# Optimization experiments

Measured on AMD Instinct MI355X. Metric: run time of the kernel, lower is better.

The kernel has to match this reference:

```python
import jax, jax.numpy as jnp
import numpy as np

V, E, H, K, VD, NH, FS, NL = 32000, 512, 512, 512, 512, 8, 2048, 6
B, MEM, SLEN = 256, 70, 11
MAXLEN = 71
THRESH = 1.0 - 0.1
EPS = 1e-6


def _timing_signal(length, channels):
    # Faithful to _gen_timing_signal (min_timescale=1, max_timescale=1e4)
    position = np.arange(length, dtype=np.float32)
    num_ts = channels // 2
    log_inc = np.log(1e4) / (num_ts - 1)
    inv_ts = np.exp(np.arange(num_ts, dtype=np.float32) * -log_inc)
    scaled = position[:, None] * inv_ts[None, :]
    sig = np.concatenate([np.sin(scaled), np.cos(scaled)], axis=1)
    return jnp.asarray(sig.reshape(1, length, channels), dtype=jnp.float32)

TIME_SIG = _timing_signal(MAXLEN, H)   # [1, 71, H]
POS_SIG = _timing_signal(NL, H)        # [1, NL, H]


def layer_norm(x, g, b):
    mu = x.mean(-1, keepdims=True)
    sd = x.std(-1, keepdims=True, ddof=1)  # torch std is unbiased
    return g * (x - mu) / (sd + EPS) + b


def conv1d(x, w, b):
    # x: [B,L,Cin]; w: torch layout [Cout,Cin,3]; 'both' padding -> same length
    y = jax.lax.conv_general_dilated(x, jnp.transpose(w, (2, 1, 0)), (1,), [(1, 1)],
                                     dimension_numbers=('NWC', 'WIO', 'NWC'))
    return y + b


def mha(x, wq, wk, wv, wo):
    Bx, L, _ = x.shape
    dk, dv = K // NH, VD // NH
    q = (x @ wq).reshape(Bx, L, NH, dk).transpose(0, 2, 1, 3) * dk ** -0.5
    k = (x @ wk).reshape(Bx, L, NH, dk).transpose(0, 2, 1, 3)
    v = (x @ wv).reshape(Bx, L, NH, dv).transpose(0, 2, 1, 3)
    a = jax.nn.softmax(jnp.einsum('bhqd,bhkd->bhqk', q, k), axis=-1)
    ctx = jnp.einsum('bhqk,bhkd->bhqd', a, v).transpose(0, 2, 1, 3).reshape(Bx, L, VD)
    return ctx @ wo


def enc_layer(x, p):
    xn = layer_norm(x, p['ln1_g'], p['ln1_b'])
    x = x + mha(xn, p['wq'], p['wk'], p['wv'], p['wo'])
    xn = layer_norm(x, p['ln2_g'], p['ln2_b'])
    y = conv1d(jax.nn.relu(conv1d(xn, p['c1_w'], p['c1_b'])), p['c2_w'], p['c2_b'])
    return x + y


def act_encode(x, p):
    Bx, L, _ = x.shape
    hp = jnp.zeros((Bx, L), x.dtype)
    rem = jnp.zeros((Bx, L), x.dtype)
    nu = jnp.zeros((Bx, L), x.dtype)
    prev = jnp.zeros_like(x)

    def step(carry, t):
        state, prev, hp, rem, nu = carry
        active = jnp.any((hp < THRESH) & (nu < NL))  # while-loop condition
        s = state + TIME_SIG[:, :L, :] + POS_SIG[:, t, :][:, None, :]
        pr = jax.nn.sigmoid(s @ p['p_w'] + p['p_b'])[..., 0]  # [B,L]
        still = (hp < 1.0).astype(x.dtype)
        tot = hp + pr * still
        new_halted = (tot > THRESH).astype(x.dtype) * still
        still2 = (tot <= THRESH).astype(x.dtype) * still
        hp2 = hp + pr * still2
        rem2 = rem + new_halted * (1.0 - hp2)
        hp2 = hp2 + new_halted * rem2
        nu2 = nu + still2 + new_halted
        uw = (pr * still2 + new_halted * rem2)[..., None]
        s2 = enc_layer(s, p)
        prev2 = s2 * uw + prev * (1.0 - uw)
        new = (s2, prev2, hp2, rem2, nu2)
        carry = jax.tree_util.tree_map(lambda a, b: jnp.where(active, b, a), carry, new)
        return carry, None

    (_, prev, hp, rem, nu), _ = jax.lax.scan(step, (x, prev, hp, rem, nu), jnp.arange(NL))
    return prev, rem, nu


def setup_inputs() -> dict:
    key = jax.random.key(0)
    ks = jax.random.split(key, 16)
    s = 0.02
    emb = jax.random.normal(ks[0], (V, E), jnp.float32) * s
    emb = emb.at[0].set(0.0)  # padding_idx=0
    return {
        'story': jax.random.randint(ks[1], (B, MEM, SLEN), 0, V),
        'query': jax.random.randint(ks[2], (B, SLEN), 0, V),
        'emb': emb,
        'mask_p': jnp.ones((11, E), jnp.float32),
        'proj_w': jax.random.normal(ks[3], (E, H), jnp.float32) * s,
        'ln1_g': jnp.ones((H,), jnp.float32), 'ln1_b': jnp.zeros((H,), jnp.float32),
        'wq': jax.random.normal(ks[4], (H, K), jnp.float32) * s,
        'wk': jax.random.normal(ks[5], (H, K), jnp.float32) * s,
        'wv': jax.random.normal(ks[6], (H, VD), jnp.float32) * s,
        'wo': jax.random.normal(ks[7], (VD, H), jnp.float32) * s,
        'c1_w': jax.random.normal(ks[8], (FS, H, 3), jnp.float32) * s,
        'c1_b': jnp.zeros((FS,), jnp.float32),
        'c2_w': jax.random.normal(ks[9], (H, FS, 3), jnp.float32) * s,
        'c2_b': jnp.zeros((H,), jnp.float32),
        'ln2_g': jnp.ones((H,), jnp.float32), 'ln2_b': jnp.zeros((H,), jnp.float32),
        'p_w': jax.random.normal(ks[10], (H, 1), jnp.float32) * s,
        'p_b': jnp.ones((1,), jnp.float32),  # bias init to 1 as in ACT_basic
        'out_b': jnp.zeros((V,), jnp.float32),
    }


def reference(story, query, emb, mask_p, proj_w, ln1_g, ln1_b, wq, wk, wv, wo,
              c1_w, c1_b, c2_w, c2_b, ln2_g, ln2_b, p_w, p_b, out_b):
    p = dict(ln1_g=ln1_g, ln1_b=ln1_b, wq=wq, wk=wk, wv=wv, wo=wo,
             c1_w=c1_w, c1_b=c1_b, c2_w=c2_w, c2_b=c2_b,
             ln2_g=ln2_g, ln2_b=ln2_b, p_w=p_w, p_b=p_b)
    S = story.shape[2]
    e = emb[story]                                         # [B,M,S,E]
    embed_story = jnp.sum(e * mask_p[:S][None, None], 2)   # [B,M,E]
    qe = emb[query]                                        # [B,S,E]
    embed_query = jnp.sum(qe[:, None] * mask_p[:query.shape[1]], 2)  # [B,1,E]
    x = jnp.concatenate([embed_story, embed_query], axis=1)          # [B,M+1,E]
    h = x @ proj_w  # proj_flag path (embedding_size == hidden_size)
    logit, rem, nu = act_encode(h, p)
    pooled = jnp.sum(logit, axis=1) / logit.shape[1]
    a_hat = pooled @ emb.T + out_b  # tied output weights
    return a_hat, jax.nn.softmax(a_hat, axis=1), rem, nu
```

## Files before the change

### kernel.cpp

```cpp
#include <hip/hip_runtime.h>
#include <hip/hip_bf16.h>
#include <math.h>


typedef unsigned short ushort_t;
using short8   = __attribute__((ext_vector_type(8))) short;
using floatx4  = __attribute__((ext_vector_type(4))) float;
using ushort4v = __attribute__((ext_vector_type(4))) unsigned short;

#define B_   256
#define L_   71
#define H_   512
#define M_   (B_*L_)
#define MH_  9088
#define FS_  2048
#define V_   32000
#define NH_  8
#define DK_  64

#define ATS  68
#define SST  72

__device__ inline ushort_t f2bf_rne(float f) {
    unsigned u = __float_as_uint(f);
    return (ushort_t)((u + 0x7FFFu + ((u >> 16) & 1u)) >> 16);
}

__device__ __forceinline__ void gload16(const void* g, void* l)
{
    __builtin_amdgcn_global_load_lds(
        (__attribute__((address_space(1))) unsigned int*)(g),
        (__attribute__((address_space(3))) unsigned int*)(l),
        16, 0, 0);
}

template<int MODE>
__global__ __launch_bounds__(256) void gemm_conv(
    const ushort_t* __restrict__ AH, const ushort_t* __restrict__ AL,
    int lda, int rowA, int rowG,
    const ushort_t* __restrict__ Bh, const ushort_t* __restrict__ Bl,
    int N, const float* __restrict__ bias,
    ushort_t* __restrict__ CoutH, ushort_t* __restrict__ CoutL,
    float* __restrict__ Cpart, long partStride, int cLen)
{
    __shared__ __attribute__((aligned(16))) short Ahs[4608], Als[4608];
    __shared__ __attribute__((aligned(16))) short Bhs[6144], Bls[6144];

    const int tid  = threadIdx.x;
    const int w    = tid >> 6, lane = tid & 63;

    int bn, by, z;
    if (MODE == 1) {
        const int id = blockIdx.x;
        const int l  = (id & 7) * 142 + (id >> 3);
        const int gp = l >> 2;
        by = gp % 71;
        const int zz = gp / 71;
        z  = zz >> 1;
        bn = (zz & 1) * 4 + (l & 3);
    } else {
        bn = blockIdx.x; by = blockIdx.y; z = 0;
    }
    const int cBeg = z * cLen;
    const int bm = by << 7;

    const int srow = lane & 15, skc = lane >> 4;
    const long aOff0 = (long)(rowA + bm - 1 + (w    ) * 16 + srow) * lda + skc * 8;
    const long aOff1 = (long)(rowA + bm - 1 + (w + 4) * 16 + srow) * lda + skc * 8;
    const long aOff2 = (long)(rowA + bm - 1 + 128 + srow) * lda + skc * 8;
    const long ldb = 3L * lda;
    const long bOff0 = (long)(bn * 64 + ((w    ) & 3) * 16 + srow) * ldb + ((w    ) >> 2) * lda + skc * 8;
    const long bOff1 = (long)(bn * 64 + ((w + 4) & 3) * 16 + srow) * ldb + ((w + 4) >> 2) * lda + skc * 8;
    const long bOff2 = (long)(bn * 64 + ((w + 8) & 3) * 16 + srow) * ldb + ((w + 8) >> 2) * lda + skc * 8;

    const int quad = lane >> 4, mr = lane & 15;
    const int boffL = quad * 128 + mr * 8;
    int aoffs[2][3];
    bool am0[2], am2[2];
    #pragma unroll
    for (int i = 0; i < 2; i++) {
        #pragma unroll
        for (int d = 0; d < 3; d++) {
            const int s = w * 32 + i * 16 + mr + d;
            aoffs[i][d] = (s >> 4) * 512 + quad * 128 + (s & 15) * 8;
        }
        const int lm = (bm + w * 32 + i * 16 + mr + rowG) % 71;
        am0[i] = (lm == 0);
        am2[i] = (lm == 70);
    }

    floatx4 acc[2][4] = {};

    const int cEnd = cBeg + cLen;
    for (int c0 = cBeg; c0 < cEnd; c0 += 32) {
        __syncthreads();
        gload16(AH + aOff0 + c0, Ahs + (w    ) * 512);
        gload16(AH + aOff1 + c0, Ahs + (w + 4) * 512);
        gload16(AL + aOff0 + c0, Als + (w    ) * 512);
        gload16(AL + aOff1 + c0, Als + (w + 4) * 512);
        if (w == 0) {
            gload16(AH + aOff2 + c0, Ahs + 8 * 512);
            gload16(AL + aOff2 + c0, Als + 8 * 512);
        }
        gload16(Bh + bOff0 + c0, Bhs + (w    ) * 512);
        gload16(Bh + bOff1 + c0, Bhs + (w + 4) * 512);
        gload16(Bh + bOff2 + c0, Bhs + (w + 8) * 512);
        gload16(Bl + bOff0 + c0, Bls + (w    ) * 512);
        gload16(Bl + bOff1 + c0, Bls + (w + 4) * 512);
        gload16(Bl + bOff2 + c0, Bls + (w + 8) * 512);
        __syncthreads();

        #pragma unroll
        for (int d = 0; d < 3; d++) {
            short8 bhf[4], blf[4];
            #pragma unroll
            for (int j = 0; j < 4; j++) {
                bhf[j] = *(const short8*)(Bhs + (d * 4 + j) * 512 + boffL);
                blf[j] = *(const short8*)(Bls + (d * 4 + j) * 512 + boffL);
            }
            #pragma unroll
            for (int i = 0; i < 2; i++) {
                short8 a_h = *(const short8*)(Ahs + aoffs[i][d]);
                short8 a_l = *(const short8*)(Als + aoffs[i][d]);
                if (d == 0) { if (am0[i]) { a_h = (short8)0; a_l = (short8)0; } }
                if (d == 2) { if (am2[i]) { a_h = (short8)0; a_l = (short8)0; } }
                #pragma unroll
                for (int j = 0; j < 4; j++) {
                    acc[i][j] = __builtin_amdgcn_mfma_f32_16x16x32_bf16(a_h, bhf[j], acc[i][j], 0, 0, 0);
                    acc[i][j] = __builtin_amdgcn_mfma_f32_16x16x32_bf16(a_l, bhf[j], acc[i][j], 0, 0, 0);
                    acc[i][j] = __builtin_amdgcn_mfma_f32_16x16x32_bf16(a_h, blf[j], acc[i][j], 0, 0, 0);
                }
            }
        }
    }

    #pragma unroll
    for (int j = 0; j < 4; j++) {
        const int gcol = bn * 64 + j * 16 + mr;
        const float bv = (MODE == 0) ? bias[gcol] : 0.f;
        #pragma unroll
        for (int i = 0; i < 2; i++) {
            #pragma unroll
            for (int r = 0; r < 4; r++) {
                const int grow = bm + w * 32 + i * 16 + quad * 4 + r;
                float v = acc[i][j][r];
                if (MODE == 0) {
                    v = fmaxf(v + bv, 0.f);
                    const long cidx = (long)grow * N + gcol;
                    ushort_t h = f2bf_rne(v);
                    float hf = __uint_as_float(((unsigned)h) << 16);
                    CoutH[cidx] = h;
                    CoutL[cidx] = f2bf_rne(v - hf);
                } else {
                    Cpart[(long)z * partStride + (long)grow * N + gcol] = v;
                }
            }
        }
    }
}

template<int TN>
__global__ __launch_bounds__(256) void gemm_s(
    const ushort_t* __restrict__ AH, const ushort_t* __restrict__ AL,
    int lda, int rowA,
    const ushort_t* __restrict__ Bh, const ushort_t* __restrict__ Bl,
    int N, int K,
    const float* __restrict__ bias, const float* residual,
    float alpha, int rowC, int outMode,
    float* Cout, ushort_t* CoutH, ushort_t* CoutL)
{
    constexpr int AF = (TN == 128) ? 4 : 2;
    __shared__ __attribute__((aligned(16))) short Ahs[4096], Als[4096];
    __shared__ __attribute__((aligned(16))) short Bhs[TN * 32], Bls[TN * 32];

    const int tid  = threadIdx.x;
    const int w    = tid >> 6, lane = tid & 63;
    const int bm = blockIdx.y << 7, bn = blockIdx.x * TN;

    const int srow = lane & 15;
    const int skc  = lane >> 4;
    const int ra0  = w * 16 + srow;
    const int ra1  = ra0 + 64;
    const ushort_t* pAh0 = AH + (long)(bm + ra0 + rowA) * lda + skc * 8;
    const ushort_t* pAl0 = AL + (long)(bm + ra0 + rowA) * lda + skc * 8;
    const ushort_t* pAh1 = AH + (long)(bm + ra1 + rowA) * lda + skc * 8;
    const ushort_t* pAl1 = AL + (long)(bm + ra1 + rowA) * lda + skc * 8;
    const ushort_t* pBh0 = Bh + (long)(bn + ra0) * K + skc * 8;
    const ushort_t* pBl0 = Bl + (long)(bn + ra0) * K + skc * 8;
    const ushort_t* pBh1 = (TN == 128) ? (Bh + (long)(bn + ra1) * K + skc * 8) : nullptr;
    const ushort_t* pBl1 = (TN == 128) ? (Bl + (long)(bn + ra1) * K + skc * 8) : nullptr;

    const int quad = lane >> 4, mr = lane & 15;
    const int wrM   = (TN == 128) ? ((w >> 1) << 6) : (w << 5);
    const int wcN   = (TN == 128) ? ((w & 1) << 6) : 0;
    const int agrp0 = (TN == 128) ? ((w >> 1) << 2) : (w << 1);
    const int bgrp0 = (TN == 128) ? ((w & 1) << 2) : 0;
    const int foff  = quad * 128 + mr * 8;

    floatx4 acc[AF][4] = {};

    for (int k0 = 0; k0 < K; k0 += 32) {
        __syncthreads();
        gload16(pAh0 + k0, Ahs + w * 512);
        gload16(pAh1 + k0, Ahs + (w + 4) * 512);
        gload16(pAl0 + k0, Als + w * 512);
        gload16(pAl1 + k0, Als + (w + 4) * 512);
        if constexpr (TN == 128) {
            gload16(pBh0 + k0, Bhs + w * 512);
            gload16(pBh1 + k0, Bhs + (w + 4) * 512);
            gload16(pBl0 + k0, Bls + w * 512);
            gload16(pBl1 + k0, Bls + (w + 4) * 512);
        } else {
            gload16(pBh0 + k0, Bhs + w * 512);
            gload16(pBl0 + k0, Bls + w * 512);
        }
        __syncthreads();

        short8 ah[AF], al[AF], bh[4], bl[4];
        #pragma unroll
        for (int i = 0; i < AF; i++) {
            ah[i] = *(const short8*)(Ahs + (agrp0 + i) * 512 + foff);
            al[i] = *(const short8*)(Als + (agrp0 + i) * 512 + foff);
        }
        #pragma unroll
        for (int j = 0; j < 4; j++) {
            bh[j] = *(const short8*)(Bhs + (bgrp0 + j) * 512 + foff);
            bl[j] = *(const short8*)(Bls + (bgrp0 + j) * 512 + foff);
        }
        #pragma unroll
        for (int i = 0; i < AF; i++)
        #pragma unroll
        for (int j = 0; j < 4; j++) {
            acc[i][j] = __builtin_amdgcn_mfma_f32_16x16x32_bf16(ah[i], bh[j], acc[i][j], 0, 0, 0);
            acc[i][j] = __builtin_amdgcn_mfma_f32_16x16x32_bf16(al[i], bh[j], acc[i][j], 0, 0, 0);
            acc[i][j] = __builtin_amdgcn_mfma_f32_16x16x32_bf16(ah[i], bl[j], acc[i][j], 0, 0, 0);
        }
    }

    #pragma unroll
    for (int j = 0; j < 4; j++) {
        const int gcol = bn + wcN + j * 16 + mr;
        const float bv = bias ? bias[gcol] : 0.f;
        #pragma unroll
        for (int i = 0; i < AF; i++) {
            #pragma unroll
            for (int r = 0; r < 4; r++) {
                const int grow = bm + wrM + i * 16 + quad * 4 + r;
                const long crow = (long)grow + rowC;
                float v = acc[i][j][r] * alpha + bv;
                if (residual) v += residual[crow * N + gcol];
                const long cidx = crow * (long)N + gcol;
                if (outMode == 2) {
                    ushort_t h = f2bf_rne(v);
                    float hf = __uint_as_float(((unsigned)h) << 16);
                    CoutH[cidx] = h;
                    CoutL[cidx] = f2bf_rne(v - hf);
                } else {
                    Cout[cidx] = v;
                }
            }
        }
    }
}

__global__ __launch_bounds__(256) void conv2_reduce(
    const float* __restrict__ part, long partStride,
    const float* __restrict__ bias, float* __restrict__ trunk,
    float* __restrict__ prev, const float* __restrict__ uw, int rowC)
{
    const long n4 = (long)MH_ * H_ / 4;
    long i4 = (long)blockIdx.x * 256 + threadIdx.x;
    if (i4 >= n4) return;
    const long row  = i4 >> 7;
    const float4 p0 = ((const float4*)part)[i4];
    const float4 p1 = ((const float4*)(part + partStride))[i4];
    const float4 b4 = ((const float4*)bias)[i4 & 127];
    const long  ti  = (long)rowC * 128 + i4;
    float4 tv = ((const float4*)trunk)[ti];
    float4 v;
    v.x = p0.x + p1.x + b4.x + tv.x;
    v.y = p0.y + p1.y + b4.y + tv.y;
    v.z = p0.z + p1.z + b4.z + tv.z;
    v.w = p0.w + p1.w + b4.w + tv.w;
    ((float4*)trunk)[ti] = v;
    const float u = uw[rowC + row];
    float4 pv = ((const float4*)prev)[ti];
    pv.x = v.x * u + pv.x * (1.f - u);
    pv.y = v.y * u + pv.y * (1.f - u);
    pv.z = v.z * u + pv.z * (1.f - u);
    pv.w = v.w * u + pv.w * (1.f - u);
    ((float4*)prev)[ti] = pv;
}

__global__ __launch_bounds__(256) void sig_prep(float* __restrict__ T, float* __restrict__ P)
{
    int i = blockIdx.x * 256 + threadIdx.x;
    const int NT = 71 * 512;
    if (i >= NT + 6 * 512) return;
    int pos, c, idx;
    float* dst;
    if (i < NT) { pos = i >> 9; c = i & 511; dst = T; idx = i; }
    else        { int j = i - NT; pos = j >> 9; c = j & 511; dst = P; idx = j; }
    const float loginc = 0.036119766f;
    int jj = c & 255;
    float inv = expf(-(float)jj * loginc);
    float arg = (float)pos * inv;
    dst[idx] = (c < 256) ? sinf(arg) : cosf(arg);
}

__global__ __launch_bounds__(256) void gate_kernel(
    const float* __restrict__ hp, const float* __restrict__ nu, int* __restrict__ flag)
{
    int i = blockIdx.x * 256 + threadIdx.x;
    bool act = (i < M_) && (hp[i] < 0.9f) && (nu[i] < 6.0f);
    unsigned long long b = __ballot(act);
    if ((threadIdx.x & 63) == 0 && b) atomicOr(flag, 1);
}

__global__ __launch_bounds__(256) void s_pr_kernel(
    float* trunk, const float* __restrict__ Ttab, const float* __restrict__ Ptab,
    const float* __restrict__ p_w, const float* __restrict__ p_b,
    float* __restrict__ hp, float* __restrict__ rem, float* __restrict__ nu,
    float* __restrict__ uw, const int* __restrict__ flag, int t)
{
    const int row  = blockIdx.x * 4 + (threadIdx.x >> 6);
    const int lane = threadIdx.x & 63;
    const int l    = row % 71;
    float dot = 0.f;
    #pragma unroll
    for (int j = 0; j < 8; j++) {
        int c  = lane + 64 * j;
        float sv = trunk[(long)row * H_ + c] + Ttab[l * H_ + c] + Ptab[t * H_ + c];
        trunk[(long)row * H_ + c] = sv;
        dot += sv * p_w[c];
    }
    #pragma unroll
    for (int o = 32; o; o >>= 1) dot += __shfl_xor(dot, o);
    if (lane == 0) {
        if (flag[0]) {
            float pr = 1.f / (1.f + expf(-(dot + p_b[0])));
            float hp0 = hp[row], rem0 = rem[row], nu0 = nu[row];
            float still = (hp0 < 1.0f) ? 1.f : 0.f;
            float tot   = hp0 + pr * still;
            float nh    = ((tot > 0.9f) ? 1.f : 0.f) * still;
            float st2   = ((tot <= 0.9f) ? 1.f : 0.f) * still;
            float hp2   = hp0 + pr * st2;
            float rem2  = rem0 + nh * (1.f - hp2);
            hp2 += nh * rem2;
            hp[row] = hp2; rem[row] = rem2; nu[row] = nu0 + st2 + nh;
            uw[row] = pr * st2 + nh * rem2;
        } else {
            uw[row] = 0.f;
        }
    }
}

__global__ __launch_bounds__(256) void ln_kernel(
    const float* __restrict__ X, const float* __restrict__ g,
    const float* __restrict__ bb, ushort_t* __restrict__ outH,
    ushort_t* __restrict__ outL)
{
    const int row  = blockIdx.x * 4 + (threadIdx.x >> 6);
    const int lane = threadIdx.x & 63;
    const float* xr = X + (long)row * H_;
    float v[8];
    float s = 0.f;
    #pragma unroll
    for (int j = 0; j < 8; j++) { v[j] = xr[lane + 64 * j]; s += v[j]; }
    #pragma unroll
    for (int o = 32; o; o >>= 1) s += __shfl_xor(s, o);
    float mean = s * (1.f / 512.f);
    float q = 0.f;
    #pragma unroll
    for (int j = 0; j < 8; j++) { float d = v[j] - mean; q += d * d; }
    #pragma unroll
    for (int o = 32; o; o >>= 1) q += __shfl_xor(q, o);
    float sd  = sqrtf(q * (1.f / 511.f));
    float inv = 1.f / (sd + 1e-6f);
    #pragma unroll
    for (int j = 0; j < 8; j++) {
        int c = lane + 64 * j;
        float val = g[c] * (v[j] - mean) * inv + bb[c];
        ushort_t h = f2bf_rne(val);
        float hf = __uint_as_float(((unsigned)h) << 16);
        long idx = (long)row * H_ + c;
        outH[idx] = h;
        outL[idx] = f2bf_rne(val - hf);
    }
}

__global__ __launch_bounds__(256) void attn_kernel(
    const float* __restrict__ qkv, ushort_t* __restrict__ ctxH,
    ushort_t* __restrict__ ctxL)
{
    __shared__ __attribute__((aligned(16))) float qs[L_ * ATS];
    __shared__ __attribute__((aligned(16))) float ks[(L_ + 1) * ATS];
    __shared__ __attribute__((aligned(16))) float Ss[L_ * SST];
    __shared__ float rsum[L_ + 1];
    const int tid = threadIdx.x;
    const int b = blockIdx.x >> 3, h = blockIdx.x & 7;
    const long qbase = (long)b * L_ * 1536 + h * DK_;

    for (int idx = tid; idx < L_ * 16; idx += 256) {
        const int i = idx >> 4, s4 = idx & 15;
        const float4 qv = *(const float4*)(qkv + qbase + (long)i * 1536 + 4 * s4);
        const float4 kv = *(const float4*)(qkv + qbase + 512 + (long)i * 1536 + 4 * s4);
        *(float4*)(qs + i * ATS + 4 * s4) = qv;
        *(float4*)(ks + i * ATS + 4 * s4) = kv;
    }
    if (tid < 16) {
        float4 zz = {0.f, 0.f, 0.f, 0.f};
        *(float4*)(ks + 71 * ATS + 4 * tid) = zz;
    }
    __syncthreads();

    for (int item = tid; item < 18 * L_; item += 256) {
        const int jq = item / 71, i = item - jq * 71;
        const float* qr = qs + i * ATS;
        const float* k0 = ks + (4 * jq) * ATS;
        float s0 = 0.f, s1 = 0.f, s2 = 0.f, s3 = 0.f;
        #pragma unroll
        for (int s4 = 0; s4 < 16; s4++) {
            const float4 qv = *(const float4*)(qr + 4 * s4);
            const float4 k0v = *(const float4*)(k0 + 4 * s4);
            const float4 k1v = *(const float4*)(k0 + ATS + 4 * s4);
            const float4 k2v = *(const float4*)(k0 + 2 * ATS + 4 * s4);
            const float4 k3v = *(const float4*)(k0 + 3 * ATS + 4 * s4);
            s0 += qv.x * k0v.x + qv.y * k0v.y + qv.z * k0v.z + qv.w * k0v.w;
            s1 += qv.x * k1v.x + qv.y * k1v.y + qv.z * k1v.z + qv.w * k1v.w;
            s2 += qv.x * k2v.x + qv.y * k2v.y + qv.z * k2v.z + qv.w * k2v.w;
            s3 += qv.x * k3v.x + qv.y * k3v.y + qv.z * k3v.z + qv.w * k3v.w;
        }
        float4 sv; sv.x = s0; sv.y = s1; sv.z = s2; sv.w = s3;
        *(float4*)(Ss + i * SST + 4 * jq) = sv;
    }
    __syncthreads();

    for (int idx = tid; idx < L_ * 16; idx += 256) {
        const int i = idx >> 4, s4 = idx & 15;
        *(float4*)(ks + i * ATS + 4 * s4) =
            *(const float4*)(qkv + qbase + 1024 + (long)i * 1536 + 4 * s4);
    }

    {
        const int g = tid >> 2, r = tid & 3;
        #pragma unroll
        for (int half = 0; half < 2; half++) {
            const int row = g + half * 64;
            if (row < L_) {
                float4 vals[5];
                float mx = -1e30f;
                #pragma unroll
                for (int t = 0; t < 5; t++) {
                    const int q = r + 4 * t;
                    if (q < 18) {
                        float4 v = *(const float4*)(Ss + row * SST + 4 * q);
                        if (q == 17) v.w = -1e30f;
                        vals[t] = v;
                        mx = fmaxf(mx, fmaxf(fmaxf(v.x, v.y), fmaxf(v.z, v.w)));
                    }
                }
                mx = fmaxf(mx, __shfl_xor(mx, 1));
                mx = fmaxf(mx, __shfl_xor(mx, 2));
                float sm = 0.f;
                #pragma unroll
                for (int t = 0; t < 5; t++) {
                    const int q = r + 4 * t;
                    if (q < 18) {
                        float4 v = vals[t];
                        v.x = expf(v.x - mx); v.y = expf(v.y - mx);
                        v.z = expf(v.z - mx); v.w = expf(v.w - mx);
                        sm += v.x + v.y + v.z + v.w;
                        *(float4*)(Ss + row * SST + 4 * q) = v;
                    }
                }
                sm += __shfl_xor(sm, 1);
                sm += __shfl_xor(sm, 2);
                if (r == 0) rsum[row] = 1.f / sm;
            }
        }
    }
    __syncthreads();

    const long obase = (long)b * L_ * H_ + h * DK_;
    for (int item = tid; item < L_ * 16; item += 256) {
        const int i = item >> 4, dq = item & 15;
        const float* sr = Ss + i * SST;
        float ax = 0.f, ay = 0.f, az = 0.f, aw = 0.f;
        #pragma unroll
        for (int jq = 0; jq < 18; jq++) {
            const float4 sv = *(const float4*)(sr + 4 * jq);
            const float* v0 = ks + (4 * jq) * ATS + 4 * dq;
            const float4 va = *(const float4*)(v0);
            const float4 vb = *(const float4*)(v0 + ATS);
            const float4 vc = *(const float4*)(v0 + 2 * ATS);
            const float4 vd = *(const float4*)(v0 + 3 * ATS);
            ax += sv.x * va.x + sv.y * vb.x + sv.z * vc.x + sv.w * vd.x;
            ay += sv.x * va.y + sv.y * vb.y + sv.z * vc.y + sv.w * vd.y;
            az += sv.x * va.z + sv.y * vb.z + sv.z * vc.z + sv.w * vd.z;
            aw += sv.x * va.w + sv.y * vb.w + sv.z * vc.w + sv.w * vd.w;
        }
        const float rs = rsum[i];
        float o[4] = {ax * rs, ay * rs, az * rs, aw * rs};
        ushort4v hv, lv;
        #pragma unroll
        for (int c = 0; c < 4; c++) {
            ushort_t hh = f2bf_rne(o[c]);
            float hf = __uint_as_float(((unsigned)hh) << 16);
            hv[c] = hh;
            lv[c] = f2bf_rne(o[c] - hf);
        }
        const long oo = obase + (long)i * H_ + 4 * dq;
        *(ushort4v*)(ctxH + oo) = hv;
        *(ushort4v*)(ctxL + oo) = lv;
    }
}

__global__ __launch_bounds__(256) void embed_kernel(
    const int* __restrict__ story, const int* __restrict__ query,
    const float* __restrict__ emb, const float* __restrict__ mask,
    ushort_t* __restrict__ xH, ushort_t* __restrict__ xL)
{
    __shared__ int idx[11];
    const int row = blockIdx.x;
    const int b = row / 71, m = row % 71;
    const int tid = threadIdx.x;
    if (tid < 11)
        idx[tid] = (m < 70) ? story[((long)b * 70 + m) * 11 + tid]
                            : query[(long)b * 11 + tid];
    __syncthreads();
    for (int c = tid; c < H_; c += 256) {
        float acc = 0.f;
        #pragma unroll
        for (int s = 0; s < 11; s++)
            acc += emb[(long)idx[s] * H_ + c] * mask[s * H_ + c];
        ushort_t h = f2bf_rne(acc);
        float hf = __uint_as_float(((unsigned)h) << 16);
        long o = (long)row * H_ + c;
        xH[o] = h;
        xL[o] = f2bf_rne(acc - hf);
    }
}

__global__ __launch_bounds__(256) void wsplitT_kernel(
    const float* __restrict__ in, ushort_t* __restrict__ hi, ushort_t* __restrict__ lo,
    int R, int C, int rowOff, float scale)
{
    long i = (long)blockIdx.x * 256 + threadIdx.x;
    if (i < (long)R * C) {
        int r = (int)(i / C), c = (int)(i % C);
        float f = in[i] * scale;
        ushort_t h = f2bf_rne(f);
        float hf = __uint_as_float(((unsigned)h) << 16);
        hi[(long)(c + rowOff) * R + r] = h;
        lo[(long)(c + rowOff) * R + r] = f2bf_rne(f - hf);
    }
}

__global__ __launch_bounds__(256) void convw_split_kernel(
    const float* __restrict__ w, ushort_t* __restrict__ hi, ushort_t* __restrict__ lo,
    int N, int C)
{
    long i = (long)blockIdx.x * 256 + threadIdx.x;
    if (i < (long)N * C * 3) {
        int n = (int)(i / (3 * C));
        int r = (int)(i % (3 * C));
        int d = r / C, c = r % C;
        float f = w[((long)n * C + c) * 3 + d];
        ushort_t h = f2bf_rne(f);
        float hf = __uint_as_float(((unsigned)h) << 16);
        hi[i] = h;
        lo[i] = f2bf_rne(f - hf);
    }
}

__global__ __launch_bounds__(256) void esplit_kernel(
    const float* __restrict__ in, ushort_t* __restrict__ hi, ushort_t* __restrict__ lo,
    long n)
{
    long i = (long)blockIdx.x * 256 + threadIdx.x;
    if (i < n) {
        float f = in[i];
        ushort_t h = f2bf_rne(f);
        float hf = __uint_as_float(((unsigned)h) << 16);
        hi[i] = h;
        lo[i] = f2bf_rne(f - hf);
    }
}

__global__ __launch_bounds__(256) void zero_f32(float* __restrict__ p, long n)
{
    long i = (long)blockIdx.x * 256 + threadIdx.x;
    if (i < n) p[i] = 0.f;
}

__global__ __launch_bounds__(256) void pooled_kernel(
    const float* __restrict__ prev, ushort_t* __restrict__ pH, ushort_t* __restrict__ pL)
{
    int i = blockIdx.x * 256 + threadIdx.x;
    int b = i >> 9, c = i & 511;
    float s = 0.f;
    for (int l = 0; l < L_; l++) s += prev[((long)b * L_ + l) * H_ + c];
    float p = s / 71.0f;
    ushort_t h = f2bf_rne(p);
    float hf = __uint_as_float(((unsigned)h) << 16);
    pH[i] = h;
    pL[i] = f2bf_rne(p - hf);
}

__global__ __launch_bounds__(256) void softmax_kernel(
    const float* __restrict__ ah, float* __restrict__ out)
{
    __shared__ float red[256];
    const int b = blockIdx.x, tid = threadIdx.x;
    const float* a = ah + (long)b * V_;
    float mx = -1e30f;
    for (int i = tid; i < V_; i += 256) mx = fmaxf(mx, a[i]);
    red[tid] = mx; __syncthreads();
    for (int o = 128; o; o >>= 1) { if (tid < o) red[tid] = fmaxf(red[tid], red[tid + o]); __syncthreads(); }
    mx = red[0]; __syncthreads();
    float s = 0.f;
    for (int i = tid; i < V_; i += 256) s += expf(a[i] - mx);
    red[tid] = s; __syncthreads();
    for (int o = 128; o; o >>= 1) { if (tid < o) red[tid] += red[tid + o]; __syncthreads(); }
    float inv = 1.f / red[0];
    float* o_ = out + (long)b * V_;
    for (int i = tid; i < V_; i += 256) o_[i] = expf(a[i] - mx) * inv;
}

__global__ __launch_bounds__(256) void tails_kernel(
    const float* __restrict__ rem, const float* __restrict__ nu, float* __restrict__ out)
{
    int i = blockIdx.x * 256 + threadIdx.x;
    if (i < M_) {
        out[i] = rem[i];
        out[M_ + i] = nu[i];
    }
}

extern "C" void kernel_launch(void* const* d_in, const int* in_sizes, int n_in,
                              void* d_out, int out_size, void* d_ws, size_t ws_size,
                              hipStream_t stream)
{
    const int*   story  = (const int*)d_in[0];
    const int*   query  = (const int*)d_in[1];
    const float* emb    = (const float*)d_in[2];
    const float* mask_p = (const float*)d_in[3];
    const float* proj_w = (const float*)d_in[4];
    const float* ln1_g  = (const float*)d_in[5];
    const float* ln1_b  = (const float*)d_in[6];
    const float* wq     = (const float*)d_in[7];
    const float* wk     = (const float*)d_in[8];
    const float* wv     = (const float*)d_in[9];
    const float* wo     = (const float*)d_in[10];
    const float* c1_w   = (const float*)d_in[11];
    const float* c1_b   = (const float*)d_in[12];
    const float* c2_w   = (const float*)d_in[13];
    const float* c2_b   = (const float*)d_in[14];
    const float* ln2_g  = (const float*)d_in[15];
    const float* ln2_b  = (const float*)d_in[16];
    const float* p_w    = (const float*)d_in[17];
    const float* p_b    = (const float*)d_in[18];
    const float* out_b  = (const float*)d_in[19];
    float* outp = (float*)d_out;

    char* wsb = (char*)d_ws;
    size_t off = 0;
    auto alloc = [&](size_t bytes) -> void* {
        void* p = wsb + off;
        off = (off + bytes + 255) & ~(size_t)255;
        return p;
    };
    const long ROWE = (long)M_ * H_;

    float* trunkF = (float*)alloc(ROWE * 4);
    float* prevF  = (float*)alloc(ROWE * 4);
    char*  poolC  = (char*)alloc(4L * ROWE * 4);
    float* hpF    = (float*)alloc((long)M_ * 4 * 4 + 64);
    float* remF   = hpF + M_;
    float* nuF    = hpF + 2 * M_;
    float* uwF    = hpF + 3 * M_;
    int*   flags  = (int*)(hpF + 4 * M_);
    ushort_t* projH = (ushort_t*)alloc((long)H_ * H_ * 2);
    ushort_t* projL = (ushort_t*)alloc((long)H_ * H_ * 2);
    ushort_t* wqkvH = (ushort_t*)alloc((long)3 * H_ * H_ * 2);
    ushort_t* wqkvL = (ushort_t*)alloc((long)3 * H_ * H_ * 2);
    ushort_t* woH   = (ushort_t*)alloc((long)H_ * H_ * 2);
    ushort_t* woL   = (ushort_t*)alloc((long)H_ * H_ * 2);
    ushort_t* W1H   = (ushort_t*)alloc((long)FS_ * 3 * H_ * 2);
    ushort_t* W1L   = (ushort_t*)alloc((long)FS_ * 3 * H_ * 2);
    ushort_t* W2H   = (ushort_t*)alloc((long)H_ * 3 * FS_ * 2);
    ushort_t* W2L   = (ushort_t*)alloc((long)H_ * 3 * FS_ * 2);
    ushort_t* pooledH = (ushort_t*)alloc((long)B_ * H_ * 2);
    ushort_t* pooledL = (ushort_t*)alloc((long)B_ * H_ * 2);
    float* Ttab     = (float*)alloc((long)L_ * H_ * 4);
    float* Ptab     = (float*)alloc(6L * H_ * 4);

    ushort_t* xnH = (ushort_t*)poolC;
    ushort_t* xnL = xnH + ROWE;
    float* qkvF = (float*)(poolC + ROWE * 4);
    ushort_t* ctxH = xnH;
    ushort_t* ctxL = xnL;
    ushort_t* xn2H = (ushort_t*)poolC;
    ushort_t* xn2L = xn2H + ROWE;
    ushort_t* y1H  = (ushort_t*)(poolC + ROWE * 4);
    ushort_t* y1L  = y1H + (long)MH_ * FS_;
    float* partF   = (float*)(poolC + ROWE * 4 + (long)MH_ * FS_ * 4);
    ushort_t* xembH = (ushort_t*)poolC;
    ushort_t* xembL = xembH + ROWE;
    ushort_t* embH = (ushort_t*)poolC;
    ushort_t* embL = embH + (long)V_ * H_;

    dim3 blk(256);

    zero_f32<<<dim3((unsigned)((ROWE + 255) / 256)), blk, 0, stream>>>(prevF, ROWE);
    zero_f32<<<dim3((3 * M_ + 255) / 256), blk, 0, stream>>>(hpF, 3 * M_);
    zero_f32<<<dim3(1), blk, 0, stream>>>((float*)flags, 16);
    sig_prep<<<dim3(154), blk, 0, stream>>>(Ttab, Ptab);

    wsplitT_kernel<<<dim3(1024), blk, 0, stream>>>(proj_w, projH, projL, H_, H_, 0, 1.f);
    wsplitT_kernel<<<dim3(1024), blk, 0, stream>>>(wq, wqkvH, wqkvL, H_, H_, 0, 0.125f);
    wsplitT_kernel<<<dim3(1024), blk, 0, stream>>>(wk, wqkvH, wqkvL, H_, H_, 512, 1.f);
    wsplitT_kernel<<<dim3(1024), blk, 0, stream>>>(wv, wqkvH, wqkvL, H_, H_, 1024, 1.f);
    wsplitT_kernel<<<dim3(1024), blk, 0, stream>>>(wo, woH, woL, H_, H_, 0, 1.f);
    convw_split_kernel<<<dim3(12288), blk, 0, stream>>>(c1_w, W1H, W1L, FS_, H_);
    convw_split_kernel<<<dim3(12288), blk, 0, stream>>>(c2_w, W2H, W2L, H_, FS_);

    embed_kernel<<<dim3(M_), blk, 0, stream>>>(story, query, emb, mask_p, xembH, xembL);
    gemm_s<64><<<dim3(H_ / 64, M_ / 128), blk, 0, stream>>>(
        xembH, xembL, H_, 0, projH, projL, H_, H_,
        nullptr, nullptr, 1.f, 0, 0, trunkF, nullptr, nullptr);

    for (int t = 0; t < 6; t++) {
        gate_kernel<<<dim3(M_ / 256), blk, 0, stream>>>(hpF, nuF, flags + t);
        s_pr_kernel<<<dim3(M_ / 4), blk, 0, stream>>>(trunkF, Ttab, Ptab, p_w, p_b,
                                                      hpF, remF, nuF, uwF, flags + t, t);
        ln_kernel<<<dim3(M_ / 4), blk, 0, stream>>>(trunkF, ln1_g, ln1_b, xnH, xnL);
        gemm_s<128><<<dim3(1536 / 128, M_ / 128), blk, 0, stream>>>(
            xnH, xnL, H_, 0, wqkvH, wqkvL, 1536, H_,
            nullptr, nullptr, 1.f, 0, 0, qkvF, nullptr, nullptr);
        attn_kernel<<<dim3(B_ * NH_), blk, 0, stream>>>(qkvF, ctxH, ctxL);
        gemm_s<64><<<dim3(H_ / 64, M_ / 128), blk, 0, stream>>>(
            ctxH, ctxL, H_, 0, woH, woL, H_, H_,
            nullptr, trunkF, 1.f, 0, 0, trunkF, nullptr, nullptr);
        ln_kernel<<<dim3(M_ / 4), blk, 0, stream>>>(trunkF, ln2_g, ln2_b, xn2H, xn2L);
        for (int half = 0; half < 2; half++) {
            int ro = half * MH_;
            gemm_conv<0><<<dim3(32, 71), blk, 0, stream>>>(
                xn2H, xn2L, H_, ro, ro, W1H, W1L, FS_,
                c1_b, y1H, y1L, nullptr, 0, 512);
            gemm_conv<1><<<dim3(1136), blk, 0, stream>>>(
                y1H, y1L, FS_, 0, ro, W2H, W2L, H_,
                nullptr, nullptr, nullptr, partF, (long)MH_ * H_, 1024);
            conv2_reduce<<<dim3((unsigned)((long)MH_ * H_ / 4 / 256)), blk, 0, stream>>>(
                partF, (long)MH_ * H_, c2_b, trunkF, prevF, uwF, ro);
        }
    }

    pooled_kernel<<<dim3(B_ * H_ / 256), blk, 0, stream>>>(prevF, pooledH, pooledL);
    esplit_kernel<<<dim3(64000), blk, 0, stream>>>(emb, embH, embL, (long)V_ * H_);
    gemm_s<64><<<dim3(V_ / 64, B_ / 128), blk, 0, stream>>>(
        pooledH, pooledL, H_, 0, embH, embL, V_, H_,
        out_b, nullptr, 1.f, 0, 0, outp, nullptr, nullptr);
    softmax_kernel<<<dim3(B_), blk, 0, stream>>>(outp, outp + (long)B_ * V_);
    tails_kernel<<<dim3((M_ + 255) / 256), blk, 0, stream>>>(remF, nuF, outp + 2L * B_ * V_);
}
```

Baseline: 7.821 ms.

## Widen conv GEMM tile to 128x128 with 2x2 warp layout and XCD-aware block mapping

The conv-as-GEMM kernel now computes a 128-column output tile per block instead of 64, with waves laid out 2x2 (each wave covering 64 rows by 64 columns). This doubles the reuse of each staged A tile and halves the number of blocks, so less global and LDS traffic is spent per MFMA. Both modes get a 1D grid with an XCD-interleaved block-to-tile remap, which aims to improve L2 locality. In exchange, LDS for B doubles and the per-wave accumulators double, which may lower occupancy, and the smaller grid may fill the CUs less evenly.

```diff
diff --git a/kernel.cpp b/kernel.cpp
--- a/kernel.cpp
+++ b/kernel.cpp
@@ -44,7 +44,7 @@
     float* __restrict__ Cpart, long partStride, int cLen)
 {
     __shared__ __attribute__((aligned(16))) short Ahs[4608], Als[4608];
-    __shared__ __attribute__((aligned(16))) short Bhs[6144], Bls[6144];
+    __shared__ __attribute__((aligned(16))) short Bhs[12288], Bls[12288];
 
     const int tid  = threadIdx.x;
     const int w    = tid >> 6, lane = tid & 63;
@@ -52,44 +52,51 @@
     int bn, by, z;
     if (MODE == 1) {
         const int id = blockIdx.x;
+        const int l  = (id & 7) * 71 + (id >> 3);
+        by = l >> 3;
+        const int mem = l & 7;
+        z  = mem >> 2;
+        bn = mem & 3;
+    } else {
+        const int id = blockIdx.x;
         const int l  = (id & 7) * 142 + (id >> 3);
-        const int gp = l >> 2;
-        by = gp % 71;
-        const int zz = gp / 71;
-        z  = zz >> 1;
-        bn = (zz & 1) * 4 + (l & 3);
-    } else {
-        bn = blockIdx.x; by = blockIdx.y; z = 0;
+        by = l >> 4;
+        bn = l & 15;
+        z  = 0;
     }
     const int cBeg = z * cLen;
     const int bm = by << 7;
 
     const int srow = lane & 15, skc = lane >> 4;
+    const long ldb = 3L * lda;
     const long aOff0 = (long)(rowA + bm - 1 + (w    ) * 16 + srow) * lda + skc * 8;
     const long aOff1 = (long)(rowA + bm - 1 + (w + 4) * 16 + srow) * lda + skc * 8;
     const long aOff2 = (long)(rowA + bm - 1 + 128 + srow) * lda + skc * 8;
-    const long ldb = 3L * lda;
-    const long bOff0 = (long)(bn * 64 + ((w    ) & 3) * 16 + srow) * ldb + ((w    ) >> 2) * lda + skc * 8;
-    const long bOff1 = (long)(bn * 64 + ((w + 4) & 3) * 16 + srow) * ldb + ((w + 4) >> 2) * lda + skc * 8;
-    const long bOff2 = (long)(bn * 64 + ((w + 8) & 3) * 16 + srow) * ldb + ((w + 8) >> 2) * lda + skc * 8;
+    long bOffs[6];
+    #pragma unroll
+    for (int t = 0; t < 6; t++) {
+        const int u = w + 4 * t;
+        const int d = u >> 3, g = u & 7;
+        bOffs[t] = (long)(bn * 128 + g * 16 + srow) * ldb + (long)d * lda + skc * 8;
+    }
 
     const int quad = lane >> 4, mr = lane & 15;
-    const int boffL = quad * 128 + mr * 8;
-    int aoffs[2][3];
-    bool am0[2], am2[2];
-    #pragma unroll
-    for (int i = 0; i < 2; i++) {
+    const int wr = w >> 1, wc = w & 1;
+    int aoffs[4][3];
+    bool am0[4], am2[4];
+    #pragma unroll
+    for (int i = 0; i < 4; i++) {
         #pragma unroll
         for (int d = 0; d < 3; d++) {
-            const int s = w * 32 + i * 16 + mr + d;
+            const int s = wr * 64 + i * 16 + mr + d;
             aoffs[i][d] = (s >> 4) * 512 + quad * 128 + (s & 15) * 8;
         }
-        const int lm = (bm + w * 32 + i * 16 + mr + rowG) % 71;
+        const int lm = (bm + wr * 64 + i * 16 + mr + rowG) % 71;
         am0[i] = (lm == 0);
         am2[i] = (lm == 70);
     }
 
-    floatx4 acc[2][4] = {};
+    floatx4 acc[4][4] = {};
 
     const int cEnd = cBeg + cLen;
     for (int c0 = cBeg; c0 < cEnd; c0 += 32) {
@@ -102,12 +109,12 @@
             gload16(AH + aOff2 + c0, Ahs + 8 * 512);
             gload16(AL + aOff2 + c0, Als + 8 * 512);
         }
-        gload16(Bh + bOff0 + c0, Bhs + (w    ) * 512);
-        gload16(Bh + bOff1 + c0, Bhs + (w + 4) * 512);
-        gload16(Bh + bOff2 + c0, Bhs + (w + 8) * 512);
-        gload16(Bl + bOff0 + c0, Bls + (w    ) * 512);
-        gload16(Bl + bOff1 + c0, Bls + (w + 4) * 512);
-        gload16(Bl + bOff2 + c0, Bls + (w + 8) * 512);
+        #pragma unroll
+        for (int t = 0; t < 6; t++) {
+            const int u = w + 4 * t;
+            gload16(Bh + bOffs[t] + c0, Bhs + u * 512);
+            gload16(Bl + bOffs[t] + c0, Bls + u * 512);
+        }
         __syncthreads();
 
         #pragma unroll
@@ -115,11 +122,12 @@
             short8 bhf[4], blf[4];
             #pragma unroll
             for (int j = 0; j < 4; j++) {
-                bhf[j] = *(const short8*)(Bhs + (d * 4 + j) * 512 + boffL);
-                blf[j] = *(const short8*)(Bls + (d * 4 + j) * 512 + boffL);
+                const int bo = (d * 8 + wc * 4 + j) * 512 + quad * 128 + mr * 8;
+                bhf[j] = *(const short8*)(Bhs + bo);
+                blf[j] = *(const short8*)(Bls + bo);
             }
             #pragma unroll
-            for (int i = 0; i < 2; i++) {
+            for (int i = 0; i < 4; i++) {
                 short8 a_h = *(const short8*)(Ahs + aoffs[i][d]);
                 short8 a_l = *(const short8*)(Als + aoffs[i][d]);
                 if (d == 0) { if (am0[i]) { a_h = (short8)0; a_l = (short8)0; } }
@@ -136,13 +144,13 @@
 
     #pragma unroll
     for (int j = 0; j < 4; j++) {
-        const int gcol = bn * 64 + j * 16 + mr;
+        const int gcol = bn * 128 + wc * 64 + j * 16 + mr;
         const float bv = (MODE == 0) ? bias[gcol] : 0.f;
         #pragma unroll
-        for (int i = 0; i < 2; i++) {
+        for (int i = 0; i < 4; i++) {
             #pragma unroll
             for (int r = 0; r < 4; r++) {
-                const int grow = bm + w * 32 + i * 16 + quad * 4 + r;
+                const int grow = bm + wr * 64 + i * 16 + quad * 4 + r;
                 float v = acc[i][j][r];
                 if (MODE == 0) {
                     v = fmaxf(v + bv, 0.f);
@@ -746,10 +754,10 @@
         ln_kernel<<<dim3(M_ / 4), blk, 0, stream>>>(trunkF, ln2_g, ln2_b, xn2H, xn2L);
         for (int half = 0; half < 2; half++) {
             int ro = half * MH_;
-            gemm_conv<0><<<dim3(32, 71), blk, 0, stream>>>(
+            gemm_conv<0><<<dim3(1136), blk, 0, stream>>>(
                 xn2H, xn2L, H_, ro, ro, W1H, W1L, FS_,
                 c1_b, y1H, y1L, nullptr, 0, 512);
-            gemm_conv<1><<<dim3(1136), blk, 0, stream>>>(
+            gemm_conv<1><<<dim3(568), blk, 0, stream>>>(
                 y1H, y1L, FS_, 0, ro, W2H, W2L, H_,
                 nullptr, nullptr, nullptr, partF, (long)MH_ * H_, 1024);
             conv2_reduce<<<dim3((unsigned)((long)MH_ * H_ / 4 / 256)), blk, 0, stream>>>(
```

Measured after the change: 8.376 ms. 1.07x slower.
